# Optimization experiments

Measured on AMD Instinct MI355X. Metric: run time of the kernel, lower is better.

The kernel has to match this reference:

```python
import jax, jax.numpy as jnp
import numpy as np

NUM_NODES = 20000
NUM_RELATIONS = 32
HIDDEN = 128
EMB = 16
NUM_EDGES = 600000


def setup_inputs() -> dict:
    key = jax.random.key(0)
    ks = jax.random.split(key, 8)
    edge_index = jax.random.randint(ks[0], (2, NUM_EDGES), 0, NUM_NODES, dtype=jnp.int64)
    edge_type = jax.random.randint(ks[1], (NUM_EDGES,), 0, NUM_RELATIONS, dtype=jnp.int64)
    node_emb = jax.random.normal(ks[2], (NUM_NODES, EMB), dtype=jnp.float32)
    W1 = jax.random.normal(ks[3], (NUM_RELATIONS, EMB, HIDDEN), dtype=jnp.float32) * (1.0 / np.sqrt(EMB))
    root1 = jax.random.normal(ks[4], (EMB, HIDDEN), dtype=jnp.float32) * (1.0 / np.sqrt(EMB))
    b1 = jnp.zeros((HIDDEN,), dtype=jnp.float32)
    W2 = jax.random.normal(ks[5], (NUM_RELATIONS, HIDDEN, HIDDEN), dtype=jnp.float32) * (1.0 / np.sqrt(HIDDEN))
    root2 = jax.random.normal(ks[6], (HIDDEN, HIDDEN), dtype=jnp.float32) * (1.0 / np.sqrt(HIDDEN))
    b2 = jnp.zeros((HIDDEN,), dtype=jnp.float32)
    return {"edge_index": edge_index, "edge_type": edge_type, "node_emb": node_emb,
            "W1": W1, "root1": root1, "b1": b1, "W2": W2, "root2": root2, "b2": b2}


def rgcn_layer(x, edge_index, edge_type, W, root, bias):
    # PyG RGCNConv: per-relation transform, per-(dst, relation) MEAN aggregation,
    # summed over relations, plus root transform and bias.
    src, dst = edge_index[0], edge_index[1]
    # mean normalization per (dst, relation) segment
    seg = dst * NUM_RELATIONS + edge_type                      # [E]
    counts = jax.ops.segment_sum(jnp.ones(seg.shape, jnp.float32), seg,
                                 num_segments=NUM_NODES * NUM_RELATIONS)
    inv = jnp.where(counts > 0, 1.0 / counts, 0.0)
    # transform every node by every relation weight: [N, R, H]
    xr = jnp.einsum('nf,rfh->nrh', x, W)
    msg = xr[src, edge_type] * inv[seg][:, None]               # [E, H]
    agg = jax.ops.segment_sum(msg, dst, num_segments=NUM_NODES)  # [N, H]
    return agg + x @ root + bias


def reference(edge_index, edge_type, node_emb, W1, root1, b1, W2, root2, b2):
    h = rgcn_layer(node_emb, edge_index, edge_type, W1, root1, b1)
    h = jax.nn.relu(h)
    h = rgcn_layer(h, edge_index, edge_type, W2, root2, b2)
    return h
```

## Files before the change

### kernel.cpp

```cpp
#include <hip/hip_runtime.h>
#include <hip/hip_bf16.h>

#define N_NODES 20000
#define N_REL 32
#define HID 128
#define EMB 16
#define N_EDGES 600000
#define NB (N_NODES * N_REL)

typedef __attribute__((ext_vector_type(8))) short  bf8v;
typedef __attribute__((ext_vector_type(8))) unsigned short us8v;
typedef __attribute__((ext_vector_type(4))) unsigned short us4v;
typedef __attribute__((ext_vector_type(4))) float  f4v;

__device__ __forceinline__ unsigned short f2b(float f) {
    __hip_bfloat16 h = __float2bfloat16(f);
    return __builtin_bit_cast(unsigned short, h);
}
__device__ __forceinline__ float b2f(unsigned short u) {
    unsigned int x = ((unsigned int)u) << 16;
    return __builtin_bit_cast(float, x);
}

__device__ __forceinline__ void lds_barrier() {
    asm volatile("s_waitcnt lgkmcnt(0)\n\ts_barrier" ::: "memory");
}

#define V_W2  (N_REL * HID * HID / 4)
#define V_XB  (N_NODES * EMB / 4)
#define V_W1  (N_REL * EMB * HID / 4)
#define V_R1  (HID * 32 / 4)
#define V_R2  (HID * HID / 4)
#define V_HIST (N_EDGES / 2)
#define PRE_TOT (V_W2 + V_XB + V_W1 + V_R1 + V_R2 + V_HIST)

__global__ __launch_bounds__(256) void pre1_k(
    const int* __restrict__ dst, const int* __restrict__ et,
    const float* __restrict__ x, const float* __restrict__ W1,
    const float* __restrict__ root1, const float* __restrict__ W2,
    const float* __restrict__ root2,
    int* __restrict__ hist,
    unsigned short* __restrict__ xb, unsigned short* __restrict__ w1t,
    unsigned short* __restrict__ r1t, unsigned short* __restrict__ w2t,
    unsigned short* __restrict__ r2t) {
    int it = blockIdx.x * 256 + threadIdx.x;
    if (it < V_W2) {
        const int i = it * 4;
        int r = i >> 14, k = (i >> 7) & 127, n0 = i & 127;
        int kb = r * 4 + (k >> 5), q = (k >> 3) & 3, j = k & 7;
        int ct8 = n0 >> 4;
        float4 wv = *(const float4*)(W2 + i);
        unsigned short* wp = w2t + (size_t)kb * 4096 + ct8 * 512
                             + (n0 & 15) * 32 + q * 8 + j;
        wp[0]  = f2b(wv.x); wp[32] = f2b(wv.y);
        wp[64] = f2b(wv.z); wp[96] = f2b(wv.w);
        return;
    }
    it -= V_W2;
    if (it < V_XB) {
        const int i = it * 4;
        float4 xv = *(const float4*)(x + i);
        us4v v; v[0] = f2b(xv.x); v[1] = f2b(xv.y);
        v[2] = f2b(xv.z); v[3] = f2b(xv.w);
        *(us4v*)(xb + i) = v;
        return;
    }
    it -= V_XB;
    if (it < V_W1) {
        const int i = it * 4;
        int rel = i >> 11, kk = (i >> 7) & 15, n0 = i & 127;
        int kb = rel >> 1, k = ((rel & 1) << 4) + kk;
        int q = k >> 3, j = k & 7, ct8 = n0 >> 4;
        float4 wv = *(const float4*)(W1 + i);
        unsigned short* wp = w1t + kb * 4096 + ct8 * 512
                             + (n0 & 15) * 32 + q * 8 + j;
        wp[0]  = f2b(wv.x); wp[32] = f2b(wv.y);
        wp[64] = f2b(wv.z); wp[96] = f2b(wv.w);
        return;
    }
    it -= V_W1;
    if (it < V_R1) {
        const int i = it * 4;
        int k = i >> 7, n0 = i & 127;
        int q = k >> 3, j = k & 7, ct8 = n0 >> 4;
        float4 rv = (k < EMB) ? *(const float4*)(root1 + k * 128 + n0)
                              : float4{0.f, 0.f, 0.f, 0.f};
        unsigned short* wp = r1t + ct8 * 512 + (n0 & 15) * 32 + q * 8 + j;
        wp[0]  = f2b(rv.x); wp[32] = f2b(rv.y);
        wp[64] = f2b(rv.z); wp[96] = f2b(rv.w);
        return;
    }
    it -= V_R1;
    if (it < V_R2) {
        const int i = it * 4;
        int k = i >> 7, n0 = i & 127;
        int ks = k >> 5, q = (k >> 3) & 3, j = k & 7, ct8 = n0 >> 4;
        float4 rv = *(const float4*)(root2 + i);
        unsigned short* wp = r2t + (ks * 8 + ct8) * 512
                             + (n0 & 15) * 32 + q * 8 + j;
        wp[0]  = f2b(rv.x); wp[32] = f2b(rv.y);
        wp[64] = f2b(rv.z); wp[96] = f2b(rv.w);
        return;
    }
    it -= V_R2;
    if (it < V_HIST) {
        const int e = it * 2;
        int2 d2 = *(const int2*)(dst + e);
        int2 t2 = *(const int2*)(et + e);
        atomicAdd(&hist[d2.x * N_REL + t2.x], 1);
        atomicAdd(&hist[d2.y * N_REL + t2.y], 1);
    }
}

__global__ void scan1_k(const int* __restrict__ hist, int* __restrict__ binoff,
                        int* __restrict__ cursors,
                        int* __restrict__ bsum, float* __restrict__ inv) {
    __shared__ int sh[256];
    const int t = threadIdx.x;
    const int base = blockIdx.x * 1024 + t * 4;
    int4 h4 = *(const int4*)(hist + base);
    float4 iv4;
    iv4.x = h4.x > 0 ? 1.0f / h4.x : 0.0f;
    iv4.y = h4.y > 0 ? 1.0f / h4.y : 0.0f;
    iv4.z = h4.z > 0 ? 1.0f / h4.z : 0.0f;
    iv4.w = h4.w > 0 ? 1.0f / h4.w : 0.0f;
    *(float4*)(inv + base) = iv4;
    int ts = h4.x + h4.y + h4.z + h4.w;
    sh[t] = ts;
    __syncthreads();
    for (int o = 1; o < 256; o <<= 1) {
        int v = (t >= o) ? sh[t - o] : 0;
        __syncthreads();
        sh[t] += v;
        __syncthreads();
    }
    int exc = sh[t] - ts;
    int4 b4;
    b4.x = exc;
    b4.y = exc + h4.x;
    b4.z = exc + h4.x + h4.y;
    b4.w = exc + h4.x + h4.y + h4.z;
    *(int4*)(binoff + base) = b4;
    *(int4*)(cursors + base) = b4;
    if (t == 255) bsum[blockIdx.x] = sh[255];
}

__global__ void scan2_k(const int* __restrict__ bsum, int* __restrict__ bbase,
                        int* __restrict__ binoff) {
    __shared__ int sh[1024];
    const int t = threadIdx.x;
    int v = (t < 625) ? bsum[t] : 0;
    sh[t] = v;
    __syncthreads();
    for (int o = 1; o < 1024; o <<= 1) {
        int u = (t >= o) ? sh[t - o] : 0;
        __syncthreads();
        sh[t] += u;
        __syncthreads();
    }
    if (t < 625) bbase[t] = sh[t] - v;
    if (t == 625) bbase[625] = N_EDGES;
    if (t == 626) binoff[NB] = 0;
}

__global__ void scatter_k(const int* __restrict__ src, const int* __restrict__ dst,
                          const int* __restrict__ et, int* __restrict__ cursors,
                          const int* __restrict__ bbase, int* __restrict__ ssrc) {
    int it = blockIdx.x * 256 + threadIdx.x;
    if (it < 4) ssrc[N_EDGES + it] = 0;
    if (it < N_EDGES / 2) {
        const int e = it * 2;
        int2 s2 = *(const int2*)(src + e);
        int2 d2 = *(const int2*)(dst + e);
        int2 t2 = *(const int2*)(et + e);
        int b0 = d2.x * N_REL + t2.x;
        int p0 = atomicAdd(&cursors[b0], 1) + bbase[b0 >> 10];
        ssrc[p0] = s2.x;
        int b1 = d2.y * N_REL + t2.y;
        int p1 = atomicAdd(&cursors[b1], 1) + bbase[b1 >> 10];
        ssrc[p1] = s2.y;
    }
}

template<int ROWS, int ROWG, int NRC, int NIT, int KR, int OUT>
__device__ __forceinline__ void gemm_body(
    const int* __restrict__ binoff, const int* __restrict__ bbase,
    const float* __restrict__ inv, const int* __restrict__ ssrc,
    const unsigned short* __restrict__ G,
    const unsigned short* __restrict__ Bw,
    const unsigned short* __restrict__ Br,
    float* __restrict__ outf, unsigned short* __restrict__ fout,
    const float* __restrict__ bias) {

    constexpr int RG  = NRC * NIT;
    constexpr int KT  = (NRC * ROWG) / 32;
    constexpr int NCH = 256 / (ROWS * NRC);
    constexpr int CW  = ROWG / NCH;
    constexpr int CP8 = CW / 8;
    constexpr int LSS = NRC * ROWG + 8;
    constexpr int RT  = ROWS / 16;
    static_assert(NCH * CW == ROWG, "chunk covering must be exact");
    static_assert(CP8 * 8 == CW, "16B unit covering");
    static_assert(KT * 32 == NRC * ROWG, "K must be a multiple of 32");
    static_assert(ROWS * NRC * NCH == 256, "all threads gather");
    static_assert(RG == 32, "single group covers all relations");
    static_assert(RT * 16 == ROWS, "rows multiple of 16");

    __shared__ __align__(16) unsigned short As[2][ROWS * LSS];
    __shared__ int   smO[ROWS * (RG + 1)];
    __shared__ float smI[ROWS * RG];

    const int t = threadIdx.x;
    const int w = t >> 6, lane = t & 63;
    const int q = lane >> 4, m16 = lane & 15;
    const int d0 = blockIdx.x * ROWS;
    const int colb = w * 32;
    const int cb16 = colb >> 4;
    const int fo = m16 * 32 + q * 8;
    const int brow = t / (NRC * NCH);
    const int rsub = (t / NCH) % NRC;
    const int gcc  = t % NCH;
    const int mb  = brow * (RG + 1) + rsub;
    const int mbI = brow * RG + rsub;
    int uo[CP8];
#pragma unroll
    for (int j = 0; j < CP8; ++j) uo[j] = (gcc + j * NCH) * 8;
    const int lbase = brow * LSS + rsub * ROWG;

    for (int i = t; i < ROWS * (RG + 1); i += 256) {
        int row = i / (RG + 1), rr = i % (RG + 1);
        int bi = (d0 + row) * N_REL + rr;
        smO[i] = binoff[bi] + bbase[bi >> 10];
    }
    for (int i = t; i < ROWS * RG; i += 256) {
        int row = i / RG, rr = i % RG;
        smI[i] = inv[(d0 + row) * N_REL + rr];
    }
    lds_barrier();

    f4v acc[RT][2];
#pragma unroll
    for (int rt = 0; rt < RT; ++rt)
#pragma unroll
        for (int ct = 0; ct < 2; ++ct) acc[rt][ct] = f4v{0.f, 0.f, 0.f, 0.f};

    us8v gE[4][CP8];
#pragma unroll
    for (int e = 0; e < 4; ++e)
#pragma unroll
        for (int j = 0; j < CP8; ++j) gE[e][j] = us8v{};
    int sx[4] = {0, 0, 0, 0};

    {
        const int so = smO[mb], cnt = smO[mb + 1] - so;
        int s0 = ssrc[so], s1 = ssrc[so + 1], s2 = ssrc[so + 2], s3 = ssrc[so + 3];
        if (cnt >= 1) {
            const unsigned short* gp = G + (size_t)s0 * ROWG;
#pragma unroll
            for (int j = 0; j < CP8; ++j) gE[0][j] = *(const us8v*)(gp + uo[j]);
        }
        if (cnt >= 2) {
            const unsigned short* gp = G + (size_t)s1 * ROWG;
#pragma unroll
            for (int j = 0; j < CP8; ++j) gE[1][j] = *(const us8v*)(gp + uo[j]);
        }
        if (cnt >= 3) {
            const unsigned short* gp = G + (size_t)s2 * ROWG;
#pragma unroll
            for (int j = 0; j < CP8; ++j) gE[2][j] = *(const us8v*)(gp + uo[j]);
        }
        if (cnt >= 4) {
            const unsigned short* gp = G + (size_t)s3 * ROWG;
#pragma unroll
            for (int j = 0; j < CP8; ++j) gE[3][j] = *(const us8v*)(gp + uo[j]);
        }
        if (NIT > 1) {
            const int so1 = smO[mb + NRC];
            sx[0] = ssrc[so1]; sx[1] = ssrc[so1 + 1];
            sx[2] = ssrc[so1 + 2]; sx[3] = ssrc[so1 + 3];
        }
    }

    bf8v bfr[2][KT];
    {
#pragma unroll
        for (int ct = 0; ct < 2; ++ct) {
#pragma unroll
            for (int ks = 0; ks < KT; ++ks)
                bfr[ct][ks] = *(const bf8v*)(Bw + ((size_t)ks * 8 + cb16 + ct) * 512 + fo);
        }
    }

#pragma unroll 2
    for (int it = 0; it < NIT; ++it) {
        unsigned short* Ab = As[it & 1];
        {
            const int so = smO[mb + it * NRC], eo = smO[mb + it * NRC + 1];
            const int cnt = eo - so;
            const float m2 = cnt >= 2 ? 1.f : 0.f;
            const float m3 = cnt >= 3 ? 1.f : 0.f;
            const float m4 = cnt >= 4 ? 1.f : 0.f;
            float a[CW];
#pragma unroll
            for (int j = 0; j < CP8; ++j)
#pragma unroll
                for (int k = 0; k < 8; ++k)
                    a[j * 8 + k] = b2f(gE[0][j][k]) + m2 * b2f(gE[1][j][k])
                                 + m3 * b2f(gE[2][j][k]) + m4 * b2f(gE[3][j][k]);
            for (int p = so + 4; p < eo; ++p) {
                const unsigned short* gp = G + (size_t)ssrc[p] * ROWG;
#pragma unroll
                for (int j = 0; j < CP8; ++j) {
                    us8v g = *(const us8v*)(gp + uo[j]);
#pragma unroll
                    for (int k = 0; k < 8; ++k) a[j * 8 + k] += b2f(g[k]);
                }
            }
            const float iv = smI[mbI + it * NRC];
            unsigned short* wp = &Ab[lbase];
#pragma unroll
            for (int j = 0; j < CP8; ++j) {
                us8v sv;
#pragma unroll
                for (int k = 0; k < 8; ++k) sv[k] = f2b(a[j * 8 + k] * iv);
                *(us8v*)(wp + uo[j]) = sv;
            }

            if (it + 1 < NIT) {
                const int b1o = mb + (it + 1) * NRC;
                const int c1 = smO[b1o + 1] - smO[b1o];
                if (c1 >= 1) {
                    const unsigned short* gp = G + (size_t)sx[0] * ROWG;
#pragma unroll
                    for (int j = 0; j < CP8; ++j) gE[0][j] = *(const us8v*)(gp + uo[j]);
                }
                if (c1 >= 2) {
                    const unsigned short* gp = G + (size_t)sx[1] * ROWG;
#pragma unroll
                    for (int j = 0; j < CP8; ++j) gE[1][j] = *(const us8v*)(gp + uo[j]);
                }
                if (c1 >= 3) {
                    const unsigned short* gp = G + (size_t)sx[2] * ROWG;
#pragma unroll
                    for (int j = 0; j < CP8; ++j) gE[2][j] = *(const us8v*)(gp + uo[j]);
                }
                if (c1 >= 4) {
                    const unsigned short* gp = G + (size_t)sx[3] * ROWG;
#pragma unroll
                    for (int j = 0; j < CP8; ++j) gE[3][j] = *(const us8v*)(gp + uo[j]);
                }
                if (it + 2 < NIT) {
                    const int so2 = smO[mb + (it + 2) * NRC];
                    sx[0] = ssrc[so2]; sx[1] = ssrc[so2 + 1];
                    sx[2] = ssrc[so2 + 2]; sx[3] = ssrc[so2 + 3];
                }
            }
        }
        lds_barrier();

        __builtin_amdgcn_s_setprio(1);
#pragma unroll
        for (int rt = 0; rt < RT; ++rt) {
            const unsigned short* ar = &Ab[(m16 + 16 * rt) * LSS];
#pragma unroll
            for (int ks = 0; ks < KT; ++ks) {
                bf8v af = *(const bf8v*)(ar + ks * 32 + q * 8);
                acc[rt][0] = __builtin_amdgcn_mfma_f32_16x16x32_bf16(af, bfr[0][ks], acc[rt][0], 0, 0, 0);
                acc[rt][1] = __builtin_amdgcn_mfma_f32_16x16x32_bf16(af, bfr[1][ks], acc[rt][1], 0, 0, 0);
            }
        }
        __builtin_amdgcn_s_setprio(0);

        if (it + 1 < NIT) {
            const int kb0 = ((it + 1) * NRC * ROWG) >> 5;
#pragma unroll
            for (int ct = 0; ct < 2; ++ct) {
#pragma unroll
                for (int ks = 0; ks < KT; ++ks)
                    bfr[ct][ks] = *(const bf8v*)(Bw + ((size_t)(kb0 + ks) * 8 + cb16 + ct) * 512 + fo);
            }
        } else {
#pragma unroll
            for (int ct = 0; ct < 2; ++ct) {
#pragma unroll
                for (int ks = 0; ks < KR; ++ks)
                    bfr[ct][ks] = *(const bf8v*)(Br + ((size_t)ks * 8 + cb16 + ct) * 512 + fo);
            }
        }
    }

    {
#pragma unroll
        for (int rt = 0; rt < RT; ++rt) {
            const unsigned short* gr = G + (size_t)(d0 + m16 + 16 * rt) * ROWG;
#pragma unroll
            for (int ks = 0; ks < KR; ++ks) {
                bf8v af;
                if constexpr (ROWG % 32 == 0) {
                    af = *(const bf8v*)(gr + ks * 32 + q * 8);
                } else {
                    af = bf8v{0, 0, 0, 0, 0, 0, 0, 0};
                    if (ks * 32 + q * 8 + 8 <= ROWG)
                        af = *(const bf8v*)(gr + ks * 32 + q * 8);
                }
                acc[rt][0] = __builtin_amdgcn_mfma_f32_16x16x32_bf16(af, bfr[0][ks], acc[rt][0], 0, 0, 0);
                acc[rt][1] = __builtin_amdgcn_mfma_f32_16x16x32_bf16(af, bfr[1][ks], acc[rt][1], 0, 0, 0);
            }
        }
    }

    if constexpr (OUT == 1) {
#pragma unroll
        for (int ct = 0; ct < 2; ++ct) {
            const int col = colb + 16 * ct + m16;
            const float bb = bias[col];
#pragma unroll
            for (int rt = 0; rt < RT; ++rt) {
#pragma unroll
                for (int g = 0; g < 4; ++g) {
                    const int rr = 16 * rt + q * 4 + g;
                    fout[(size_t)(d0 + rr) * HID + col] =
                        f2b(fmaxf(acc[rt][ct][g] + bb, 0.0f));
                }
            }
        }
    } else {
#pragma unroll
        for (int ct = 0; ct < 2; ++ct) {
            const int col = colb + 16 * ct + m16;
            const float bb = bias[col];
#pragma unroll
            for (int rt = 0; rt < RT; ++rt) {
#pragma unroll
                for (int g = 0; g < 4; ++g) {
                    const int rr = 16 * rt + q * 4 + g;
                    outf[(size_t)(d0 + rr) * HID + col] = acc[rt][ct][g] + bb;
                }
            }
        }
    }
}

__global__ __launch_bounds__(256) void gemm_l1(
    const int* __restrict__ binoff, const int* __restrict__ bbase,
    const float* __restrict__ inv, const int* __restrict__ ssrc,
    const unsigned short* __restrict__ G, const unsigned short* __restrict__ Bw,
    const unsigned short* __restrict__ Br,
    unsigned short* __restrict__ fout, const float* __restrict__ bias) {
    gemm_body<32, 16, 4, 8, 1, 1>(binoff, bbase, inv, ssrc, G, Bw, Br,
                                  nullptr, fout, bias);
}

__global__ __launch_bounds__(256) void gemm_l2(
    const int* __restrict__ binoff, const int* __restrict__ bbase,
    const float* __restrict__ inv, const int* __restrict__ ssrc,
    const unsigned short* __restrict__ G, const unsigned short* __restrict__ Bw,
    const unsigned short* __restrict__ Br,
    float* __restrict__ outf, const float* __restrict__ bias) {
    gemm_body<32, 128, 1, 32, 4, 2>(binoff, bbase, inv, ssrc, G, Bw, Br,
                                    outf, nullptr, bias);
}

extern "C" void kernel_launch(void* const* d_in, const int* in_sizes, int n_in,
                              void* d_out, int out_size, void* d_ws, size_t ws_size,
                              hipStream_t stream) {
    const int*   ei    = (const int*)d_in[0];
    const int*   et    = (const int*)d_in[1];
    const float* x     = (const float*)d_in[2];
    const float* W1    = (const float*)d_in[3];
    const float* root1 = (const float*)d_in[4];
    const float* b1    = (const float*)d_in[5];
    const float* W2    = (const float*)d_in[6];
    const float* root2 = (const float*)d_in[7];
    const float* b2    = (const float*)d_in[8];
    float* out = (float*)d_out;

    char* ws = (char*)d_ws;
    size_t off = 0;
    auto alloc = [&](size_t bytes) { void* p = ws + off; off = (off + bytes + 63) & ~(size_t)63; return p; };
    int*   hist    = (int*)  alloc((size_t)NB * 4);
    int*   binoff  = (int*)  alloc((size_t)(NB + 1) * 4);
    int*   cursors = (int*)  alloc((size_t)NB * 4);
    float* inv     = (float*)alloc((size_t)NB * 4);
    int*   bsum    = (int*)  alloc(625 * 4);
    int*   bbase   = (int*)  alloc(626 * 4);
    int*   ssrc    = (int*)  alloc((size_t)(N_EDGES + 4) * 4);
    unsigned short* xb  = (unsigned short*)alloc((size_t)N_NODES * EMB * 2);
    unsigned short* h1b = (unsigned short*)alloc((size_t)N_NODES * HID * 2);
    unsigned short* w1t = (unsigned short*)alloc((size_t)N_REL * EMB * HID * 2);
    unsigned short* r1t = (unsigned short*)alloc((size_t)HID * 32 * 2);
    unsigned short* w2t = (unsigned short*)alloc((size_t)N_REL * HID * HID * 2);
    unsigned short* r2t = (unsigned short*)alloc((size_t)HID * HID * 2);

    const int* src = ei;
    const int* dst = ei + N_EDGES;

    hipMemsetAsync(hist, 0, (size_t)NB * 4, stream);
    pre1_k<<<(PRE_TOT + 255) / 256, 256, 0, stream>>>(
        dst, et, x, W1, root1, W2, root2, hist, xb, w1t, r1t, w2t, r2t);
    scan1_k<<<NB / 1024, 256, 0, stream>>>(hist, binoff, cursors, bsum, inv);
    scan2_k<<<1, 1024, 0, stream>>>(bsum, bbase, binoff);
    scatter_k<<<(N_EDGES / 2 + 255) / 256, 256, 0, stream>>>(src, dst, et, cursors, bbase, ssrc);

    gemm_l1<<<dim3(625, 1), 256, 0, stream>>>(
        binoff, bbase, inv, ssrc, xb, w1t, r1t, h1b, b1);

    gemm_l2<<<dim3(625, 1), 256, 0, stream>>>(
        binoff, bbase, inv, ssrc, h1b, w2t, r2t, out, b2);
}
```

Baseline: 230.4 us.

## Rewrite layer-2 fused gather-GEMM as wave-independent kernel without block barriers

Replaces the generic layer-2 template instantiation with a dedicated kernel. It uses 128-thread blocks in which each wave independently owns 16 destination rows and all 128 output columns. Each wave gathers and mean-scales its own neighbor rows into a private double-buffered LDS tile, so no block-wide barriers are needed. B fragments are streamed from global memory per relation, with loads interleaved between MFMAs. The aim is to remove cross-wave synchronization and let waves overlap their gather latency, at the cost of reloading relation weights per wave and using fewer threads per block.

After: 313.5 us. +36.1%, slower.

```diff
diff --git a/kernel.cpp b/kernel.cpp
--- a/kernel.cpp
+++ b/kernel.cpp
@@ -182,15 +182,14 @@
     }
 }
 
-template<int ROWS, int ROWG, int NRC, int NIT, int KR, int OUT>
+template<int ROWS, int ROWG, int NRC, int NIT, int KR>
 __device__ __forceinline__ void gemm_body(
     const int* __restrict__ binoff, const int* __restrict__ bbase,
     const float* __restrict__ inv, const int* __restrict__ ssrc,
     const unsigned short* __restrict__ G,
     const unsigned short* __restrict__ Bw,
     const unsigned short* __restrict__ Br,
-    float* __restrict__ outf, unsigned short* __restrict__ fout,
-    const float* __restrict__ bias) {
+    unsigned short* __restrict__ fout, const float* __restrict__ bias) {
 
     constexpr int RG  = NRC * NIT;
     constexpr int KT  = (NRC * ROWG) / 32;
@@ -199,12 +198,10 @@
     constexpr int CP8 = CW / 8;
     constexpr int LSS = NRC * ROWG + 8;
     constexpr int RT  = ROWS / 16;
-    static_assert(NCH * CW == ROWG, "chunk covering must be exact");
+    static_assert(NCH * CW == ROWG, "chunk covering");
     static_assert(CP8 * 8 == CW, "16B unit covering");
-    static_assert(KT * 32 == NRC * ROWG, "K must be a multiple of 32");
     static_assert(ROWS * NRC * NCH == 256, "all threads gather");
-    static_assert(RG == 32, "single group covers all relations");
-    static_assert(RT * 16 == ROWS, "rows multiple of 16");
+    static_assert(RG == 32, "single group");
 
     __shared__ __align__(16) unsigned short As[2][ROWS * LSS];
     __shared__ int   smO[ROWS * (RG + 1)];
@@ -282,14 +279,11 @@
     }
 
     bf8v bfr[2][KT];
-    {
-#pragma unroll
-        for (int ct = 0; ct < 2; ++ct) {
-#pragma unroll
-            for (int ks = 0; ks < KT; ++ks)
-                bfr[ct][ks] = *(const bf8v*)(Bw + ((size_t)ks * 8 + cb16 + ct) * 512 + fo);
-        }
-    }
+#pragma unroll
+    for (int ct = 0; ct < 2; ++ct)
+#pragma unroll
+        for (int ks = 0; ks < KT; ++ks)
+            bfr[ct][ks] = *(const bf8v*)(Bw + ((size_t)ks * 8 + cb16 + ct) * 512 + fo);
 
 #pragma unroll 2
     for (int it = 0; it < NIT; ++it) {
@@ -374,18 +368,16 @@
         if (it + 1 < NIT) {
             const int kb0 = ((it + 1) * NRC * ROWG) >> 5;
 #pragma unroll
-            for (int ct = 0; ct < 2; ++ct) {
+            for (int ct = 0; ct < 2; ++ct)
 #pragma unroll
                 for (int ks = 0; ks < KT; ++ks)
                     bfr[ct][ks] = *(const bf8v*)(Bw + ((size_t)(kb0 + ks) * 8 + cb16 + ct) * 512 + fo);
-            }
         } else {
 #pragma unroll
-            for (int ct = 0; ct < 2; ++ct) {
+            for (int ct = 0; ct < 2; ++ct)
 #pragma unroll
                 for (int ks = 0; ks < KR; ++ks)
                     bfr[ct][ks] = *(const bf8v*)(Br + ((size_t)ks * 8 + cb16 + ct) * 512 + fo);
-            }
         }
     }
 
@@ -395,47 +387,26 @@
             const unsigned short* gr = G + (size_t)(d0 + m16 + 16 * rt) * ROWG;
 #pragma unroll
             for (int ks = 0; ks < KR; ++ks) {
-                bf8v af;
-                if constexpr (ROWG % 32 == 0) {
+                bf8v af = bf8v{0, 0, 0, 0, 0, 0, 0, 0};
+                if (ks * 32 + q * 8 + 8 <= ROWG)
                     af = *(const bf8v*)(gr + ks * 32 + q * 8);
-                } else {
-                    af = bf8v{0, 0, 0, 0, 0, 0, 0, 0};
-                    if (ks * 32 + q * 8 + 8 <= ROWG)
-                        af = *(const bf8v*)(gr + ks * 32 + q * 8);
-                }
                 acc[rt][0] = __builtin_amdgcn_mfma_f32_16x16x32_bf16(af, bfr[0][ks], acc[rt][0], 0, 0, 0);
                 acc[rt][1] = __builtin_amdgcn_mfma_f32_16x16x32_bf16(af, bfr[1][ks], acc[rt][1], 0, 0, 0);
             }
         }
     }
 
-    if constexpr (OUT == 1) {
-#pragma unroll
-        for (int ct = 0; ct < 2; ++ct) {
-            const int col = colb + 16 * ct + m16;
-            const float bb = bias[col];
-#pragma unroll
-            for (int rt = 0; rt < RT; ++rt) {
-#pragma unroll
-                for (int g = 0; g < 4; ++g) {
-                    const int rr = 16 * rt + q * 4 + g;
-                    fout[(size_t)(d0 + rr) * HID + col] =
-                        f2b(fmaxf(acc[rt][ct][g] + bb, 0.0f));
-                }
-            }
-        }
-    } else {
-#pragma unroll
-        for (int ct = 0; ct < 2; ++ct) {
-            const int col = colb + 16 * ct + m16;
-            const float bb = bias[col];
-#pragma unroll
-            for (int rt = 0; rt < RT; ++rt) {
-#pragma unroll
-                for (int g = 0; g < 4; ++g) {
-                    const int rr = 16 * rt + q * 4 + g;
-                    outf[(size_t)(d0 + rr) * HID + col] = acc[rt][ct][g] + bb;
-                }
+#pragma unroll
+    for (int ct = 0; ct < 2; ++ct) {
+        const int col = colb + 16 * ct + m16;
+        const float bb = bias[col];
+#pragma unroll
+        for (int rt = 0; rt < RT; ++rt) {
+#pragma unroll
+            for (int g = 0; g < 4; ++g) {
+                const int rr = 16 * rt + q * 4 + g;
+                fout[(size_t)(d0 + rr) * HID + col] =
+                    f2b(fmaxf(acc[rt][ct][g] + bb, 0.0f));
             }
         }
     }
@@ -447,18 +418,188 @@
     const unsigned short* __restrict__ G, const unsigned short* __restrict__ Bw,
     const unsigned short* __restrict__ Br,
     unsigned short* __restrict__ fout, const float* __restrict__ bias) {
-    gemm_body<32, 16, 4, 8, 1, 1>(binoff, bbase, inv, ssrc, G, Bw, Br,
-                                  nullptr, fout, bias);
-}
-
-__global__ __launch_bounds__(256) void gemm_l2(
+    gemm_body<32, 16, 4, 8, 1>(binoff, bbase, inv, ssrc, G, Bw, Br, fout, bias);
+}
+
+__global__ __launch_bounds__(128) void gemm_l2w(
     const int* __restrict__ binoff, const int* __restrict__ bbase,
     const float* __restrict__ inv, const int* __restrict__ ssrc,
-    const unsigned short* __restrict__ G, const unsigned short* __restrict__ Bw,
+    const unsigned short* __restrict__ G,
+    const unsigned short* __restrict__ Bw,
     const unsigned short* __restrict__ Br,
     float* __restrict__ outf, const float* __restrict__ bias) {
-    gemm_body<32, 128, 1, 32, 4, 2>(binoff, bbase, inv, ssrc, G, Bw, Br,
-                                    outf, nullptr, bias);
+
+    constexpr int LSS = 136;
+    __shared__ __align__(16) unsigned short As[2][2][16 * LSS];
+    __shared__ int   smO[2][16 * 33];
+    __shared__ float smI[2][16 * 32];
+
+    const int lane = threadIdx.x & 63;
+    const int wv   = threadIdx.x >> 6;
+    const int q = lane >> 4, m16 = lane & 15;
+    const int d0 = blockIdx.x * 32 + wv * 16;
+    const int fo = m16 * 32 + q * 8;
+    const int brow = lane >> 2;
+    const int gcc  = lane & 3;
+    const int mb   = brow * 33;
+    int uo[4];
+#pragma unroll
+    for (int j = 0; j < 4; ++j) uo[j] = (gcc + j * 4) * 8;
+    const int lbase = brow * LSS;
+
+    for (int i = lane; i < 16 * 33; i += 64) {
+        int row = i / 33, rr = i % 33;
+        int bi = (d0 + row) * N_REL + rr;
+        smO[wv][i] = binoff[bi] + bbase[bi >> 10];
+    }
+    for (int i = lane; i < 16 * 32; i += 64) {
+        smI[wv][i] = inv[(d0 + (i >> 5)) * N_REL + (i & 31)];
+    }
+
+    f4v acc[8];
+#pragma unroll
+    for (int ct = 0; ct < 8; ++ct) acc[ct] = f4v{0.f, 0.f, 0.f, 0.f};
+
+    us8v gE[4][4];
+#pragma unroll
+    for (int e = 0; e < 4; ++e)
+#pragma unroll
+        for (int j = 0; j < 4; ++j) gE[e][j] = us8v{};
+    int sx[4] = {0, 0, 0, 0};
+
+    auto stage4 = [&](int s0, int s1, int s2, int s3, int c) __attribute__((always_inline)) {
+        if (c >= 1) {
+            const unsigned short* gp = G + (size_t)s0 * HID;
+#pragma unroll
+            for (int j = 0; j < 4; ++j) gE[0][j] = *(const us8v*)(gp + uo[j]);
+        }
+        if (c >= 2) {
+            const unsigned short* gp = G + (size_t)s1 * HID;
+#pragma unroll
+            for (int j = 0; j < 4; ++j) gE[1][j] = *(const us8v*)(gp + uo[j]);
+        }
+        if (c >= 3) {
+            const unsigned short* gp = G + (size_t)s2 * HID;
+#pragma unroll
+            for (int j = 0; j < 4; ++j) gE[2][j] = *(const us8v*)(gp + uo[j]);
+        }
+        if (c >= 4) {
+            const unsigned short* gp = G + (size_t)s3 * HID;
+#pragma unroll
+            for (int j = 0; j < 4; ++j) gE[3][j] = *(const us8v*)(gp + uo[j]);
+        }
+    };
+
+    {
+        const int so = smO[wv][mb], cnt = smO[wv][mb + 1] - so;
+        stage4(ssrc[so], ssrc[so + 1], ssrc[so + 2], ssrc[so + 3], cnt);
+        const int so1 = smO[wv][mb + 1];
+        sx[0] = ssrc[so1]; sx[1] = ssrc[so1 + 1];
+        sx[2] = ssrc[so1 + 2]; sx[3] = ssrc[so1 + 3];
+    }
+
+    for (int rel = 0; rel < N_REL; ++rel) {
+        unsigned short* Ab = &As[wv][rel & 1][0];
+        {
+            const int so = smO[wv][mb + rel], eo = smO[wv][mb + rel + 1];
+            const int cnt = eo - so;
+            const float m2 = cnt >= 2 ? 1.f : 0.f;
+            const float m3 = cnt >= 3 ? 1.f : 0.f;
+            const float m4 = cnt >= 4 ? 1.f : 0.f;
+            const float iv = smI[wv][brow * 32 + rel];
+            unsigned short* wp = &Ab[lbase];
+#pragma unroll
+            for (int j = 0; j < 4; ++j) {
+                float aj[8];
+#pragma unroll
+                for (int k = 0; k < 8; ++k)
+                    aj[k] = b2f(gE[0][j][k]) + m2 * b2f(gE[1][j][k])
+                          + m3 * b2f(gE[2][j][k]) + m4 * b2f(gE[3][j][k]);
+                for (int p = so + 4; p < eo; ++p) {
+                    const unsigned short* gp = G + (size_t)ssrc[p] * HID;
+                    us8v g = *(const us8v*)(gp + uo[j]);
+#pragma unroll
+                    for (int k = 0; k < 8; ++k) aj[k] += b2f(g[k]);
+                }
+                us8v sv;
+#pragma unroll
+                for (int k = 0; k < 8; ++k) sv[k] = f2b(aj[k] * iv);
+                *(us8v*)(wp + uo[j]) = sv;
+            }
+
+            if (rel + 1 < N_REL) {
+                const int b1o = mb + rel + 1;
+                stage4(sx[0], sx[1], sx[2], sx[3], smO[wv][b1o + 1] - smO[wv][b1o]);
+                if (rel + 2 < N_REL) {
+                    const int so2 = smO[wv][mb + rel + 2];
+                    sx[0] = ssrc[so2]; sx[1] = ssrc[so2 + 1];
+                    sx[2] = ssrc[so2 + 2]; sx[3] = ssrc[so2 + 3];
+                }
+            }
+        }
+
+        bf8v af[4];
+        {
+            const unsigned short* ar = &Ab[m16 * LSS + q * 8];
+#pragma unroll
+            for (int ks = 0; ks < 4; ++ks)
+                af[ks] = *(const bf8v*)(ar + ks * 32);
+        }
+
+        const unsigned short* Bp = Bw + (size_t)rel * 16384;
+        bf8v b0[4], b1[4];
+#pragma unroll
+        for (int ks = 0; ks < 4; ++ks)
+            b0[ks] = *(const bf8v*)(Bp + ((size_t)ks * 8 + 0) * 512 + fo);
+        __builtin_amdgcn_s_setprio(1);
+#pragma unroll
+        for (int ct = 0; ct < 8; ct += 2) {
+#pragma unroll
+            for (int ks = 0; ks < 4; ++ks)
+                b1[ks] = *(const bf8v*)(Bp + ((size_t)ks * 8 + ct + 1) * 512 + fo);
+#pragma unroll
+            for (int ks = 0; ks < 4; ++ks)
+                acc[ct] = __builtin_amdgcn_mfma_f32_16x16x32_bf16(af[ks], b0[ks], acc[ct], 0, 0, 0);
+            if (ct + 2 < 8) {
+#pragma unroll
+                for (int ks = 0; ks < 4; ++ks)
+                    b0[ks] = *(const bf8v*)(Bp + ((size_t)ks * 8 + ct + 2) * 512 + fo);
+            }
+#pragma unroll
+            for (int ks = 0; ks < 4; ++ks)
+                acc[ct + 1] = __builtin_amdgcn_mfma_f32_16x16x32_bf16(af[ks], b1[ks], acc[ct + 1], 0, 0, 0);
+        }
+        __builtin_amdgcn_s_setprio(0);
+    }
+
+    {
+        const unsigned short* gr = G + (size_t)(d0 + m16) * HID + q * 8;
+        bf8v af[4];
+#pragma unroll
+        for (int ks = 0; ks < 4; ++ks)
+            af[ks] = *(const bf8v*)(gr + ks * 32);
+        bf8v b0[4];
+#pragma unroll
+        for (int ct = 0; ct < 8; ++ct) {
+#pragma unroll
+            for (int ks = 0; ks < 4; ++ks)
+                b0[ks] = *(const bf8v*)(Br + ((size_t)ks * 8 + ct) * 512 + fo);
+#pragma unroll
+            for (int ks = 0; ks < 4; ++ks)
+                acc[ct] = __builtin_amdgcn_mfma_f32_16x16x32_bf16(af[ks], b0[ks], acc[ct], 0, 0, 0);
+        }
+    }
+
+#pragma unroll
+    for (int ct = 0; ct < 8; ++ct) {
+        const int col = ct * 16 + m16;
+        const float bb = bias[col];
+#pragma unroll
+        for (int g = 0; g < 4; ++g) {
+            const int rr = q * 4 + g;
+            outf[(size_t)(d0 + rr) * HID + col] = acc[ct][g] + bb;
+        }
+    }
 }
 
 extern "C" void kernel_launch(void* const* d_in, const int* in_sizes, int n_in,
@@ -505,6 +646,6 @@
     gemm_l1<<<dim3(625, 1), 256, 0, stream>>>(
         binoff, bbase, inv, ssrc, xb, w1t, r1t, h1b, b1);
 
-    gemm_l2<<<dim3(625, 1), 256, 0, stream>>>(
+    gemm_l2w<<<dim3(625, 1), 128, 0, stream>>>(
         binoff, bbase, inv, ssrc, h1b, w2t, r2t, out, b2);
 }
```
